# Kernel tuning notes

Hardware: AMD Instinct MI355X
Metric: run time of the kernel (lower is better)

The kernel has to match this reference:

```python
import jax, jax.numpy as jnp
import numpy as np

K = 32  # neighbors per sampled point
EPS = 1e-5

def _layernorm(h, g, b):
    mu = jnp.mean(h, axis=-1, keepdims=True)
    var = jnp.mean((h - mu) ** 2, axis=-1, keepdims=True)
    return (h - mu) * jax.lax.rsqrt(var + EPS) * g + b


def setup_inputs() -> dict:
    key = jax.random.key(0)
    ks = jax.random.split(key, 20)
    N, M, D_IN, D_T = 32768, 4096, 64, 128
    s = lambda k, *sh: jax.random.normal(k, sh, dtype=jnp.float32) * 0.05
    inp = {
        "x": jax.random.normal(ks[0], (N, D_IN), dtype=jnp.float32),
        "pos": jax.random.normal(ks[1], (N, 3), dtype=jnp.float32),
        "idx": jax.random.randint(ks[2], (M,), 0, N, dtype=jnp.int32),
        "batch": jnp.zeros((N,), dtype=jnp.int32),
        # PointNetConv MLP [67 -> 128 -> 256] (ReLU after first layer only)
        "W1": s(ks[3], D_IN + 3, 128), "b1": jnp.zeros((128,), jnp.float32),
        "W2": s(ks[4], 128, 256),     "b2": jnp.zeros((256,), jnp.float32),
        # feature_reduction Linear(256, 128)
        "Wr": s(ks[5], 256, D_T), "br": jnp.zeros((D_T,), jnp.float32),
        # MultiheadAttention(128, 4)
        "in_proj_w": s(ks[6], D_T, 3 * D_T), "in_proj_b": jnp.zeros((3 * D_T,), jnp.float32),
        "out_proj_w": s(ks[7], D_T, D_T),    "out_proj_b": jnp.zeros((D_T,), jnp.float32),
        # transformer MLP [128 -> 256 -> 128]
        "Wm1": s(ks[8], D_T, 2 * D_T), "bm1": jnp.zeros((2 * D_T,), jnp.float32),
        "Wm2": s(ks[9], 2 * D_T, D_T), "bm2": jnp.zeros((D_T,), jnp.float32),
        # layer norms
        "g1": jnp.ones((D_T,), jnp.float32), "beta1": jnp.zeros((D_T,), jnp.float32),
        "g2": jnp.ones((D_T,), jnp.float32), "beta2": jnp.zeros((D_T,), jnp.float32),
    }
    return inp


def _forward(x, pos, idx, batch, W1, b1, W2, b2, Wr, br,
             in_proj_w, in_proj_b, out_proj_w, out_proj_b,
             Wm1, bm1, Wm2, bm2, g1, beta1, g2, beta2):
    q_pos = pos[idx]                                    # [M,3]
    # KNN: k nearest source points for each sampled (dst) point
    d2 = (jnp.sum(q_pos ** 2, -1, keepdims=True)
          - 2.0 * (q_pos @ pos.T)
          + jnp.sum(pos ** 2, -1)[None, :])             # [M,N]
    _, col = jax.lax.top_k(-d2, K)                      # [M,K] source indices
    # PointNetConv message: nn([x_j, pos_j - pos_i]), max-aggregate per dst
    x_j = x[col]                                        # [M,K,64]
    rel = pos[col] - q_pos[:, None, :]                  # [M,K,3]
    feat = jnp.concatenate([x_j, rel], axis=-1)         # [M,K,67]
    h = jax.nn.relu(feat @ W1 + b1) @ W2 + b2           # [M,K,256]
    agg = jnp.max(h, axis=1)                            # [M,256]
    xt = agg @ Wr + br                                  # [M,128]
    # TransformerBlock: x.view(M,1,128) -> MHA over seq len M, batch 1
    M, D = xt.shape
    H = 4
    Dh = D // H
    qkv = xt @ in_proj_w + in_proj_b                    # [M,3D]
    qh, kh, vh = [t.reshape(M, H, Dh) for t in jnp.split(qkv, 3, axis=-1)]
    scores = jnp.einsum('qhd,khd->hqk', qh, kh) / np.sqrt(Dh)
    attn = jax.nn.softmax(scores, axis=-1)
    att = jnp.einsum('hqk,khd->qhd', attn, vh).reshape(M, D)
    att = att @ out_proj_w + out_proj_b
    xt = _layernorm(xt + att, g1, beta1)
    mlp = jax.nn.relu(xt @ Wm1 + bm1) @ Wm2 + bm2
    xt = _layernorm(xt + mlp, g2, beta2)
    return xt, q_pos, batch[idx]


def reference(x, pos, idx, batch, W1, b1, W2, b2, Wr, br,
              in_proj_w, in_proj_b, out_proj_w, out_proj_b,
              Wm1, bm1, Wm2, bm2, g1, beta1, g2, beta2):
    return _forward(x, pos, idx, batch, W1, b1, W2, b2, Wr, br,
                    in_proj_w, in_proj_b, out_proj_w, out_proj_b,
                    Wm1, bm1, Wm2, bm2, g1, beta1, g2, beta2)
```

## Files before the change

kernel.cpp:

```cpp
#include <hip/hip_runtime.h>
#include <hip/hip_bf16.h>

#define DEV static __device__ __forceinline__

typedef __attribute__((ext_vector_type(8))) short          s16x8;
typedef __attribute__((ext_vector_type(8))) unsigned short u16x8;
typedef __attribute__((ext_vector_type(4))) float          f32x4;
typedef __attribute__((ext_vector_type(4))) unsigned int   u32x4;

#define MFMA16(A,B,C) __builtin_amdgcn_mfma_f32_16x16x32_bf16((A),(B),(C),0,0,0)

DEV unsigned short f2bf(float f) {
  unsigned int u = __builtin_bit_cast(unsigned int, f);
  u += 0x7fffu + ((u >> 16) & 1u);
  return (unsigned short)(u >> 16);
}

#define QSCL 0.25503562201f

#define GRID_LO  (-5.0f)
#define GRID_IH  (3.2f)

DEV int cellc(float v) {
  int c = (int)floorf((v - GRID_LO) * GRID_IH);
  return min(31, max(0, c));
}

constexpr size_t OFF_POS4  = 0;
constexpr size_t OFF_COL   = 524288;
constexpr size_t OFF_W1T   = 1048576;
constexpr size_t OFF_W2T   = OFF_W1T  + 24576;
constexpr size_t OFF_WRT   = OFF_W2T  + 65536;
constexpr size_t OFF_WQKVT = OFF_WRT  + 65536;
constexpr size_t OFF_WOUTT = OFF_WQKVT+ 98304;
constexpr size_t OFF_WM1T  = OFF_WOUTT+ 32768;
constexpr size_t OFF_WM2T  = OFF_WM1T + 65536;
constexpr size_t OFF_H     = OFF_WM2T + 65536;
constexpr size_t OFF_SPOS    = OFF_H;
constexpr size_t OFF_CELLCNT = OFF_H + 524288;
constexpr size_t OFF_CELLDSC = OFF_H + 655360;
constexpr size_t OFF_FILL    = OFF_H + 917504;
constexpr size_t OFF_PO      = OFF_H;
constexpr size_t OFF_PL      = OFF_H + 16777216;
constexpr size_t OFF_AGG   = OFF_H    + 33554432;
constexpr size_t OFF_XT0   = OFF_AGG  + 4194304;
constexpr size_t OFF_QKV   = OFF_XT0  + 2097152;
constexpr size_t OFF_ATT   = OFF_QKV  + 6291456;
constexpr size_t OFF_PRE   = OFF_ATT  + 2097152;
constexpr size_t OFF_XT1   = OFF_PRE  + 2097152;
constexpr size_t OFF_MLP1  = OFF_XT1  + 2097152;
constexpr size_t OFF_SBIAS = OFF_MLP1 + 4194304;

__global__ __launch_bounds__(256) void zero_k(int* __restrict__ p) {
  p[blockIdx.x * 256 + threadIdx.x] = 0;
}

__global__ __launch_bounds__(256) void prep_k(
    const float* __restrict__ pos, const float* __restrict__ W1,
    const float* __restrict__ W2, const float* __restrict__ Wr,
    const float* __restrict__ ipw, const float* __restrict__ ipb,
    const float* __restrict__ opw,
    const float* __restrict__ Wm1, const float* __restrict__ Wm2,
    float4* __restrict__ pos4, unsigned short* __restrict__ w1t,
    unsigned short* __restrict__ w2t, unsigned short* __restrict__ wrt,
    unsigned short* __restrict__ wqkvt, unsigned short* __restrict__ woutt,
    unsigned short* __restrict__ wm1t, unsigned short* __restrict__ wm2t,
    int* __restrict__ cellcnt, float* __restrict__ sbias) {
  int T = blockIdx.x * 256 + threadIdx.x;
  if (T < 32768) {
    float px = pos[T*3], py = pos[T*3+1], pz = pos[T*3+2];
    pos4[T] = make_float4(px, py, pz, 0.f);
    int cid = (cellc(pz)*32 + cellc(py))*32 + cellc(px);
    atomicAdd(&cellcnt[cid], 1);
    return;
  }
  T -= 32768;
  if (T < 128*96)  { int n=T/96,  k=T%96;  w1t[T]  = f2bf(k < 67 ? W1[k*128+n] : 0.f); return; }
  T -= 128*96;
  if (T < 256*128) { int n=T/128, k=T%128; w2t[T]  = f2bf(W2[k*256+n]);  return; }
  T -= 256*128;
  if (T < 128*256) { int n=T/256, k=T%256; wrt[T]  = f2bf(Wr[k*128+n]);  return; }
  T -= 128*256;
  if (T < 384*128) { int n=T/128, k=T%128;
                     float v = ipw[k*384+n];
                     if (n < 128) v *= QSCL;
                     wqkvt[T]= f2bf(v); return; }
  T -= 384*128;
  if (T < 128*128) { int n=T/128, k=T%128; woutt[T]= f2bf(opw[k*128+n]); return; }
  T -= 128*128;
  if (T < 256*128) { int n=T/128, k=T%128; wm1t[T] = f2bf(Wm1[k*256+n]); return; }
  T -= 256*128;
  if (T < 128*256) { int n=T/256, k=T%256; wm2t[T] = f2bf(Wm2[k*128+n]); return; }
  T -= 128*256;
  if (T < 384) { sbias[T] = ipb[T] * (T < 128 ? QSCL : 1.f); return; }
}

__global__ __launch_bounds__(1024) void prefix_k(const int* __restrict__ cnt,
                                                 int2* __restrict__ desc,
                                                 int* __restrict__ fill) {
  __shared__ int wsum[16];
  const int tid = threadIdx.x, lane = tid & 63, w = tid >> 6;
  int loc[32]; int s = 0;
  #pragma unroll
  for (int i = 0; i < 32; ++i) { loc[i] = cnt[tid*32 + i]; s += loc[i]; }
  int sc = s;
  #pragma unroll
  for (int off = 1; off < 64; off <<= 1) {
    int v = __shfl_up(sc, off);
    if (lane >= off) sc += v;
  }
  if (lane == 63) wsum[w] = sc;
  __syncthreads();
  if (tid == 0) {
    int run = 0;
    #pragma unroll
    for (int i = 0; i < 16; ++i) { int v = wsum[i]; wsum[i] = run; run += v; }
  }
  __syncthreads();
  int base = wsum[w] + (sc - s);
  #pragma unroll
  for (int i = 0; i < 32; ++i) {
    int c = tid*32 + i;
    desc[c] = make_int2(base, loc[i]);
    fill[c] = base;
    base += loc[i];
  }
}

__global__ __launch_bounds__(256) void scatter_k(const float4* __restrict__ pos4,
                                                 int* __restrict__ fill,
                                                 float4* __restrict__ spos) {
  int T = blockIdx.x * 256 + threadIdx.x;
  float4 p = pos4[T];
  int cid = (cellc(p.z)*32 + cellc(p.y))*32 + cellc(p.x);
  int slot = atomicAdd(&fill[cid], 1);
  spos[slot] = make_float4(p.x, p.y, p.z, __int_as_float(T));
}

#define KNN_CAP  320
#define KNN_TRIG 192
#define KNN_KEEP 33
#define KNN_INF  3e37f

__global__ __launch_bounds__(256) void knn_k(
    const float4* __restrict__ spos, const int2* __restrict__ desc,
    const float4* __restrict__ pos4, const int* __restrict__ idx,
    int* __restrict__ col,
    float* __restrict__ outqpos, float* __restrict__ outbatch) {
  __shared__ float bufd[4][KNN_CAP];
  __shared__ int   bufi[4][KNN_CAP];
  __shared__ int   shist[4][64];
  __shared__ int2  segs[4][128];
  const int tid = threadIdx.x, lane = tid & 63, w = tid >> 6;
  const unsigned long long ltmask = (1ull << lane) - 1ull;

  const int q = blockIdx.x * 4 + w;
  const int iq = idx[q];
  const float4 qp = pos4[iq];
  const float qx = qp.x, qy = qp.y, qz = qp.z;
  const int cx0 = cellc(qx), cy0 = cellc(qy), cz0 = cellc(qz);

  float t = KNN_INF;
  int cnt = 0;

  auto compact = [&]() {
    int c_ = min(cnt, KNN_CAP);
    float vd[5]; int vi[5], bs[5]; bool okv[5];
    float dmax = 1e-30f;
    #pragma unroll
    for (int s = 0; s < 5; ++s) {
      int o2 = s*64 + lane;
      okv[s] = o2 < c_;
      vd[s] = okv[s] ? bufd[w][o2] : 0.f;
      vi[s] = okv[s] ? bufi[w][o2] : 0;
      dmax = fmaxf(dmax, vd[s]);
    }
    #pragma unroll
    for (int off = 1; off < 64; off <<= 1) dmax = fmaxf(dmax, __shfl_xor(dmax, off));
    float scale = 63.99f / dmax;
    shist[w][lane] = 0;
    #pragma unroll
    for (int s = 0; s < 5; ++s) {
      bs[s] = okv[s] ? min(63, (int)(vd[s] * scale)) : 64;
      if (okv[s]) atomicAdd(&shist[w][bs[s]], 1);
    }
    int h = shist[w][lane];
    #pragma unroll
    for (int off = 1; off < 64; off <<= 1) {
      int v = __shfl_up(h, off);
      if (lane >= off) h += v;
    }
    unsigned long long mk = __ballot(h >= KNN_KEEP);
    int E = mk ? (__ffsll((long long)mk) - 1) : 63;
    int base = 0;
    #pragma unroll
    for (int s = 0; s < 5; ++s) {
      bool keep = okv[s] && bs[s] <= E;
      unsigned long long km = __ballot(keep);
      int pp = base + (int)__popcll(km & ltmask);
      if (keep) { bufd[w][pp] = vd[s]; bufi[w][pp] = vi[s]; }
      base += (int)__popcll(km);
    }
    cnt = base;
    t = fminf(t, (float)(E + 1) / scale);
  };

  auto scan_rows = [&](int knew, int kold) {
    const int S = 2*knew + 1;
    const int NR = S*S;
    const float invS = 1.f / (float)S;
    for (int r0 = 0; r0 < NR; r0 += 64) {
      int r = r0 + lane;
      bool v = r < NR;
      int dz = (int)((float)r * invS);
      int rem = r - dz*S;
      if (rem < 0) { dz--; rem += S; } else if (rem >= S) { dz++; rem -= S; }
      int ccz = cz0 + dz - knew, ccy = cy0 + rem - knew;
      bool rowok = v && ccz >= 0 && ccz < 32 && ccy >= 0 && ccy < 32;
      bool inner = kold >= 0 && abs(dz - knew) <= kold && abs(rem - knew) <= kold;
      int cbase = (ccz*32 + ccy) * 32;
      int sL = 0, lL = 0, sR = 0, lR = 0;
      if (rowok) {
        int xa = max(cx0 - knew, 0);
        int xb = inner ? (cx0 - kold - 1) : min(cx0 + knew, 31);
        if (xa <= xb) {
          int2 d0 = desc[cbase + xa];
          int2 d1 = desc[cbase + xb];
          sL = d0.x; lL = d1.x + d1.y - d0.x;
        }
        if (inner) {
          int xa2 = cx0 + kold + 1, xb2 = min(cx0 + knew, 31);
          if (xa2 <= xb2 && xa2 >= 0) {
            int2 d0 = desc[cbase + xa2];
            int2 d1 = desc[cbase + xb2];
            sR = d0.x; lR = d1.x + d1.y - d0.x;
          }
        }
      }
      int cumL = lL;
      #pragma unroll
      for (int off = 1; off < 64; off <<= 1) {
        int vv = __shfl_up(cumL, off);
        if (lane >= off) cumL += vv;
      }
      int sumL = __shfl(cumL, 63);
      int cumR = lR;
      #pragma unroll
      for (int off = 1; off < 64; off <<= 1) {
        int vv = __shfl_up(cumR, off);
        if (lane >= off) cumR += vv;
      }
      int sumR = __shfl(cumR, 63);
      segs[w][lane]      = make_int2(sL, cumL - lL);
      segs[w][64 + lane] = make_int2(sR, sumL + cumR - lR);
      const int total = sumL + sumR;

      for (int b = 0; b < total; b += 320) {
        float d2v[5]; int piv[5]; bool hv[5];
        #pragma unroll
        for (int s5 = 0; s5 < 5; ++s5) {
          int p = b + s5*64 + lane;
          bool act = p < total;
          hv[s5] = false; d2v[s5] = 0.f; piv[s5] = 0;
          if (act) {
            int lo = 0;
            #pragma unroll
            for (int st = 64; st > 0; st >>= 1)
              if (segs[w][lo + st].y <= p) lo += st;
            int2 e = segs[w][lo];
            float4 pt = spos[e.x + (p - e.y)];
            float ddx = qx-pt.x, ddy = qy-pt.y, ddz = qz-pt.z;
            float d2 = ddx*ddx + ddy*ddy + ddz*ddz;
            d2v[s5] = d2; piv[s5] = __float_as_int(pt.w);
            hv[s5] = d2 < t;
          }
        }
        #pragma unroll
        for (int s5 = 0; s5 < 5; ++s5) {
          unsigned long long hm = __ballot(hv[s5]);
          if (hm) {
            int pp = cnt + (int)__popcll(hm & ltmask);
            if (hv[s5] && pp < KNN_CAP) { bufd[w][pp] = d2v[s5]; bufi[w][pp] = piv[s5]; }
            cnt += (int)__popcll(hm);
            if (cnt >= KNN_TRIG) compact();
          }
        }
      }
    }
  };

  auto bound32 = [&]() -> float {
    int c_ = min(cnt, KNN_CAP);
    float vv[5]; bool okv[5];
    float dmax = 1e-30f;
    #pragma unroll
    for (int s = 0; s < 5; ++s) {
      int o2 = s*64 + lane;
      okv[s] = o2 < c_;
      vv[s] = okv[s] ? bufd[w][o2] : 0.f;
      dmax = fmaxf(dmax, vv[s]);
    }
    #pragma unroll
    for (int off = 1; off < 64; off <<= 1) dmax = fmaxf(dmax, __shfl_xor(dmax, off));
    float scale = 63.99f / dmax;
    shist[w][lane] = 0;
    #pragma unroll
    for (int s = 0; s < 5; ++s)
      if (okv[s]) atomicAdd(&shist[w][min(63, (int)(vv[s] * scale))], 1);
    int h = shist[w][lane];
    #pragma unroll
    for (int off = 1; off < 64; off <<= 1) {
      int v = __shfl_up(h, off);
      if (lane >= off) h += v;
    }
    unsigned long long m = __ballot(h >= 32);
    int E = m ? (__ffsll((long long)m) - 1) : 63;
    return (float)(E + 1) / scale;
  };

  int kcur = 1;
  scan_rows(1, -1);
  for (int it = 0; it < 64; ++it) {
    if (cnt >= 32) {
      float t32u = bound32();
      t = fminf(t, t32u);
      int kneed = (int)(__builtin_sqrtf(t32u) * GRID_IH) + 1;
      if (kneed <= kcur || kcur >= 31) break;
      int knew = min(kneed, 31);
      scan_rows(knew, kcur);
      kcur = knew;
    } else {
      if (kcur >= 31) break;
      int knew = min(kcur + (cnt == 0 ? 2 : 1), 31);
      scan_rows(knew, kcur);
      kcur = knew;
    }
  }

  {
    int c_ = min(cnt, KNN_CAP);
    float vd[5]; int vi[5], bs[5]; bool okf[5];
    float dmax = 1e-30f;
    #pragma unroll
    for (int s = 0; s < 5; ++s) {
      int o2 = s*64 + lane;
      okf[s] = o2 < c_;
      vd[s] = okf[s] ? bufd[w][o2] : KNN_INF;
      vi[s] = okf[s] ? bufi[w][o2] : 0;
      dmax = fmaxf(dmax, okf[s] ? vd[s] : 0.f);
    }
    #pragma unroll
    for (int off = 1; off < 64; off <<= 1) dmax = fmaxf(dmax, __shfl_xor(dmax, off));
    float sc64 = 63.99f / dmax;
    shist[w][lane] = 0;
    #pragma unroll
    for (int s = 0; s < 5; ++s) {
      bs[s] = okf[s] ? min(63, (int)(vd[s] * sc64)) : 64;
      if (okf[s]) atomicAdd(&shist[w][bs[s]], 1);
    }
    int h = shist[w][lane];
    #pragma unroll
    for (int off = 1; off < 64; off <<= 1) {
      int v = __shfl_up(h, off);
      if (lane >= off) h += v;
    }
    unsigned long long m = __ballot(h >= 32);
    int E = m ? (__ffsll((long long)m) - 1) : 63;
    int c0 = (E > 0) ? __shfl(h, E - 1) : 0;
    int base = 0;
    #pragma unroll
    for (int s = 0; s < 5; ++s) {
      bool wr = okf[s] && (bs[s] < E);
      unsigned long long km = __ballot(wr);
      int pp = base + (int)__popcll(km & ltmask);
      if (wr) col[q*32 + pp] = vi[s];
      base += (int)__popcll(km);
    }
    #pragma unroll
    for (int s = 0; s < 5; ++s)
      if (!(okf[s] && bs[s] == E)) vd[s] = KNN_INF;
    int r = 32 - c0;
    #pragma unroll 1
    for (int kk = 0; kk < r; ++kk) {
      float bd = vd[0]; int bi = vi[0]; int bc = lane*8;
      #pragma unroll
      for (int s = 1; s < 5; ++s)
        if (vd[s] < bd) { bd = vd[s]; bi = vi[s]; bc = lane*8 + s; }
      #pragma unroll
      for (int off = 1; off < 64; off <<= 1) {
        float od = __shfl_xor(bd, off);
        int   oi = __shfl_xor(bi, off);
        int   oc = __shfl_xor(bc, off);
        if (od < bd || (od == bd && oc < bc)) { bd = od; bi = oi; bc = oc; }
      }
      if ((bc >> 3) == lane) {
        int sl = bc & 7;
        #pragma unroll
        for (int s = 0; s < 5; ++s) if (sl == s) vd[s] = KNN_INF;
      }
      if (lane == 0) col[q*32 + c0 + kk] = bi;
    }
  }
  if (lane == 0) {
    outqpos[q*3+0] = qx; outqpos[q*3+1] = qy; outqpos[q*3+2] = qz;
    outbatch[q] = 0.f;
  }
}

#define LA1(r,c) S[(r)*104 + (c)]
#define LB1(r,c) S[13312 + (r)*104 + (c)]
#define HB(r,c)  S[(r)*136 + (c)]
#define W2C(r,c) S[17408 + (r)*136 + (c)]

__global__ __launch_bounds__(256) void conv_k(
    const float* __restrict__ x, const float4* __restrict__ pos4,
    const int* __restrict__ idx, const int* __restrict__ col,
    const unsigned short* __restrict__ w1t, const float* __restrict__ b1,
    const unsigned short* __restrict__ w2t, const float* __restrict__ b2,
    float* __restrict__ agg) {
  __shared__ __align__(16) unsigned short S[26624];
  __shared__ int   sci[128];
  __shared__ float sqp[4][3];
  const int tid = threadIdx.x, lane = tid & 63, w = tid >> 6;
  const int wm = w >> 1, wn = w & 1;
  const int m0 = blockIdx.x * 4;

  if (tid < 128) sci[tid] = col[m0*32 + tid];
  if (tid >= 128 && tid < 132) {
    int m = m0 + tid - 128;
    float4 p = pos4[idx[m]];
    sqp[tid-128][0] = p.x; sqp[tid-128][1] = p.y; sqp[tid-128][2] = p.z;
  }
  #pragma unroll
  for (int rnd = 0; rnd < 6; ++rnd) {
    int e = (rnd*256 + tid) * 8;
    int n = e / 96, k = e % 96;
    *(u16x8*)&LB1(n, k) = *(const u16x8*)&w1t[e];
  }
  __syncthreads();

  {
    int r = tid >> 1, half = tid & 1;
    int ci = sci[r];
    const float* src = x + (size_t)ci*64 + half*32;
    #pragma unroll
    for (int c = 0; c < 4; ++c) {
      float4 va = ((const float4*)src)[c*2], vb = ((const float4*)src)[c*2+1];
      u16x8 v;
      v[0]=f2bf(va.x); v[1]=f2bf(va.y); v[2]=f2bf(va.z); v[3]=f2bf(va.w);
      v[4]=f2bf(vb.x); v[5]=f2bf(vb.y); v[6]=f2bf(vb.z); v[7]=f2bf(vb.w);
      *(u16x8*)&LA1(r, half*32 + c*8) = v;
    }
  }
  if (tid < 128) {
    int r = tid, g = r >> 5;
    float4 p = pos4[sci[r]];
    u16x8 z;
    #pragma unroll
    for (int e = 0; e < 8; ++e) z[e] = 0;
    u16x8 v0 = z;
    v0[0] = f2bf(p.x - sqp[g][0]); v0[1] = f2bf(p.y - sqp[g][1]); v0[2] = f2bf(p.z - sqp[g][2]);
    *(u16x8*)&LA1(r, 64) = v0;
    #pragma unroll
    for (int c = 1; c < 5; ++c) *(u16x8*)&LA1(r, 64 + c*8) = z;
  }
  __syncthreads();

  f32x4 acc[4][4];
  #pragma unroll
  for (int nf = 0; nf < 4; ++nf) {
    float bv = b1[wn*64 + nf*16 + (lane & 15)];
    #pragma unroll
    for (int mf = 0; mf < 4; ++mf) acc[mf][nf] = f32x4{bv, bv, bv, bv};
  }
  #pragma unroll
  for (int kc = 0; kc < 3; ++kc) {
    s16x8 af[4], bf_[4];
    #pragma unroll
    for (int mf = 0; mf < 4; ++mf)
      af[mf] = *(const s16x8*)&LA1(wm*64 + mf*16 + (lane&15), kc*32 + (lane>>4)*8);
    #pragma unroll
    for (int nf = 0; nf < 4; ++nf)
      bf_[nf] = *(const s16x8*)&LB1(wn*64 + nf*16 + (lane&15), kc*32 + (lane>>4)*8);
    #pragma unroll
    for (int mf = 0; mf < 4; ++mf)
      #pragma unroll
      for (int nf = 0; nf < 4; ++nf)
        acc[mf][nf] = MFMA16(af[mf], bf_[nf], acc[mf][nf]);
  }
  __syncthreads();

  #pragma unroll
  for (int mf = 0; mf < 4; ++mf)
    #pragma unroll
    for (int nf = 0; nf < 4; ++nf)
      #pragma unroll
      for (int j = 0; j < 4; ++j) {
        int rloc = wm*64 + mf*16 + ((lane>>4)<<2) + j;
        int cloc = wn*64 + nf*16 + (lane & 15);
        HB(rloc, cloc) = f2bf(fmaxf(acc[mf][nf][j], 0.f));
      }
  {
    int r2 = tid >> 2, kq = (tid & 3) * 32;
    const unsigned short* src = w2t + (size_t)r2*128 + kq;
    #pragma unroll
    for (int c = 0; c < 4; ++c)
      *(u16x8*)&W2C(r2, kq + c*8) = *(const u16x8*)&src[c*8];
  }
  __syncthreads();

  #pragma unroll 1
  for (int nc = 0; nc < 4; ++nc) {
    f32x4 acc2[2][4];
    #pragma unroll
    for (int nf = 0; nf < 4; ++nf) {
      float bv = b2[nc*64 + nf*16 + (lane & 15)];
      acc2[0][nf] = f32x4{bv, bv, bv, bv};
      acc2[1][nf] = f32x4{bv, bv, bv, bv};
    }
    #pragma unroll
    for (int ks = 0; ks < 4; ++ks) {
      s16x8 af[2], bf_[4];
      #pragma unroll
      for (int mf = 0; mf < 2; ++mf)
        af[mf] = *(const s16x8*)&HB(w*32 + mf*16 + (lane&15), ks*32 + (lane>>4)*8);
      #pragma unroll
      for (int nf = 0; nf < 4; ++nf)
        bf_[nf] = *(const s16x8*)&W2C(nf*16 + (lane&15), ks*32 + (lane>>4)*8);
      #pragma unroll
      for (int mf = 0; mf < 2; ++mf)
        #pragma unroll
        for (int nf = 0; nf < 4; ++nf)
          acc2[mf][nf] = MFMA16(af[mf], bf_[nf], acc2[mf][nf]);
    }
    #pragma unroll
    for (int nf = 0; nf < 4; ++nf) {
      float mx = acc2[0][nf][0];
      #pragma unroll
      for (int j = 1; j < 4; ++j) mx = fmaxf(mx, acc2[0][nf][j]);
      #pragma unroll
      for (int j = 0; j < 4; ++j) mx = fmaxf(mx, acc2[1][nf][j]);
      mx = fmaxf(mx, __shfl_xor(mx, 16));
      mx = fmaxf(mx, __shfl_xor(mx, 32));
      if (lane < 16) agg[(size_t)(m0 + w)*256 + nc*64 + nf*16 + lane] = mx;
    }
    if (nc < 3) {
      __syncthreads();
      int r2 = tid >> 2, kq = (tid & 3) * 32;
      const unsigned short* src = w2t + (size_t)((nc+1)*64 + r2)*128 + kq;
      #pragma unroll
      for (int c = 0; c < 4; ++c)
        *(u16x8*)&W2C(r2, kq + c*8) = *(const u16x8*)&src[c*8];
      __syncthreads();
    }
  }
}

template<int KFULL, int NFULL, bool RELU, bool HAS_RES, bool OBF16>
__global__ __launch_bounds__(256) void gemm_k(
    const float* __restrict__ A, const unsigned short* __restrict__ Bt,
    const float* __restrict__ bias, const float* __restrict__ res,
    float* __restrict__ out) {
  __shared__ unsigned short lA[64][72];
  __shared__ unsigned short lB[64][72];
  const int tid = threadIdx.x, lane = tid & 63, w = tid >> 6;
  const int m0 = blockIdx.x * 64, n0 = blockIdx.y * 64;

  f32x4 acc[4];
  #pragma unroll
  for (int nf = 0; nf < 4; ++nf) {
    float bv = bias[n0 + nf*16 + (lane & 15)];
    acc[nf] = f32x4{bv, bv, bv, bv};
  }

  for (int kb = 0; kb < KFULL; kb += 64) {
    __syncthreads();
    {
      int r = tid >> 2, kq = (tid & 3) * 16;
      const float* src = A + (size_t)(m0 + r)*KFULL + kb + kq;
      #pragma unroll
      for (int c = 0; c < 2; ++c) {
        float4 va = ((const float4*)src)[c*2], vb = ((const float4*)src)[c*2+1];
        u16x8 v;
        v[0]=f2bf(va.x); v[1]=f2bf(va.y); v[2]=f2bf(va.z); v[3]=f2bf(va.w);
        v[4]=f2bf(vb.x); v[5]=f2bf(vb.y); v[6]=f2bf(vb.z); v[7]=f2bf(vb.w);
        *(u16x8*)&lA[r][kq + c*8] = v;
      }
      const unsigned short* srcb = Bt + (size_t)(n0 + r)*KFULL + kb + kq;
      #pragma unroll
      for (int c = 0; c < 2; ++c)
        *(u16x8*)&lB[r][kq + c*8] = *(const u16x8*)&srcb[c*8];
    }
    __syncthreads();
    #pragma unroll
    for (int ks = 0; ks < 2; ++ks) {
      s16x8 af = *(const s16x8*)&lA[w*16 + (lane&15)][ks*32 + (lane>>4)*8];
      s16x8 bf_[4];
      #pragma unroll
      for (int nf = 0; nf < 4; ++nf)
        bf_[nf] = *(const s16x8*)&lB[nf*16 + (lane&15)][ks*32 + (lane>>4)*8];
      #pragma unroll
      for (int nf = 0; nf < 4; ++nf)
        acc[nf] = MFMA16(af, bf_[nf], acc[nf]);
    }
  }
  #pragma unroll
  for (int nf = 0; nf < 4; ++nf)
    #pragma unroll
    for (int j = 0; j < 4; ++j) {
      int row = m0 + w*16 + ((lane>>4)<<2) + j;
      int colg = n0 + nf*16 + (lane & 15);
      float v = acc[nf][j];
      if (HAS_RES) v += res[(size_t)row*NFULL + colg];
      if (RELU)    v = fmaxf(v, 0.f);
      if (OBF16) ((unsigned short*)out)[(size_t)row*NFULL + colg] = f2bf(v);
      else       out[(size_t)row*NFULL + colg] = v;
    }
}

__global__ __launch_bounds__(256) void attn_k(
    const unsigned short* __restrict__ qkvb,
    float* __restrict__ po, float* __restrict__ pl) {
  __shared__ unsigned short lK[128][40];
  __shared__ unsigned short lV[32][136];
  const int tid = threadIdx.x, lane = tid & 63, w = tid >> 6;
  const int hh = blockIdx.y, sp = blockIdx.z;
  const int qr = blockIdx.x * 64 + w * 16;
  const int g = lane >> 4, q = lane & 15;

  s16x8 qf = *(const s16x8*)&qkvb[(size_t)(qr + q)*384 + hh*32 + g*8];

  f32x4 o[2];
  o[0] = f32x4{0.f,0.f,0.f,0.f}; o[1] = f32x4{0.f,0.f,0.f,0.f};
  float lrun = 0.f;

  const int srcA = q | ((2*(g & 1)) << 4);
  const int srcB = srcA + 16;
  const bool hi = (g >> 1) != 0;

  for (int kt = sp*4; kt < sp*4 + 4; ++kt) {
    const int k0 = kt * 128;
    __syncthreads();
    {
      int key = tid >> 1, d0 = (tid & 1) * 16;
      const unsigned short* src = qkvb + (size_t)(k0 + key)*384 + 128 + hh*32 + d0;
      *(u16x8*)&lK[key][d0]     = *(const u16x8*)&src[0];
      *(u16x8*)&lK[key][d0 + 8] = *(const u16x8*)&src[8];
    }
    {
      int kp = tid & 63, gg = tid >> 6;
      const unsigned short* s0 = qkvb + (size_t)(k0 + 2*kp)*384 + 256 + hh*32 + gg*8;
      u16x8 e0 = *(const u16x8*)s0;
      u16x8 e1 = *(const u16x8*)(s0 + 384);
      #pragma unroll
      for (int d = 0; d < 8; ++d) {
        unsigned int pkk = (unsigned int)e0[d] | ((unsigned int)e1[d] << 16);
        *(unsigned int*)&lV[gg*8 + d][2*kp] = pkk;
      }
    }
    __syncthreads();

    unsigned int pk[8][2];
    float ps = 0.f;
    #pragma unroll
    for (int nf = 0; nf < 8; ++nf) {
      s16x8 kf = *(const s16x8*)&lK[nf*16 + q][g*8];
      f32x4 c = MFMA16(kf, qf, (f32x4{0.f,0.f,0.f,0.f}));
      float p0 = exp2f(c[0]), p1 = exp2f(c[1]);
      float p2 = exp2f(c[2]), p3 = exp2f(c[3]);
      ps += (p0 + p1) + (p2 + p3);
      unsigned int u0 = __builtin_bit_cast(unsigned int, p0) + 0x8000u;
      unsigned int u1 = __builtin_bit_cast(unsigned int, p1) + 0x8000u;
      unsigned int u2 = __builtin_bit_cast(unsigned int, p2) + 0x8000u;
      unsigned int u3 = __builtin_bit_cast(unsigned int, p3) + 0x8000u;
      pk[nf][0] = (u0 >> 16) | (u1 & 0xffff0000u);
      pk[nf][1] = (u2 >> 16) | (u3 & 0xffff0000u);
    }
    ps += __shfl_xor(ps, 16);
    ps += __shfl_xor(ps, 32);
    lrun += ps;

    #pragma unroll
    for (int kc = 0; kc < 4; ++kc) {
      unsigned int a0 = (unsigned int)__shfl((int)pk[2*kc][0],   srcA);
      unsigned int b0 = (unsigned int)__shfl((int)pk[2*kc+1][0], srcA);
      unsigned int a1 = (unsigned int)__shfl((int)pk[2*kc][1],   srcA);
      unsigned int b1 = (unsigned int)__shfl((int)pk[2*kc+1][1], srcA);
      unsigned int a2 = (unsigned int)__shfl((int)pk[2*kc][0],   srcB);
      unsigned int b2 = (unsigned int)__shfl((int)pk[2*kc+1][0], srcB);
      unsigned int a3 = (unsigned int)__shfl((int)pk[2*kc][1],   srcB);
      unsigned int b3 = (unsigned int)__shfl((int)pk[2*kc+1][1], srcB);
      u32x4 wv;
      wv[0] = hi ? b0 : a0; wv[1] = hi ? b1 : a1;
      wv[2] = hi ? b2 : a2; wv[3] = hi ? b3 : a3;
      s16x8 pa = __builtin_bit_cast(s16x8, wv);
      #pragma unroll
      for (int df = 0; df < 2; ++df) {
        s16x8 vf = *(const s16x8*)&lV[df*16 + q][kc*32 + g*8];
        o[df] = MFMA16(pa, vf, o[df]);
      }
    }
  }
  #pragma unroll
  for (int df = 0; df < 2; ++df)
    #pragma unroll
    for (int j = 0; j < 4; ++j) {
      int row = qr + g*4 + j;
      po[((size_t)sp*4096 + row)*128 + hh*32 + df*16 + q] = o[df][j];
    }
  if (lane < 16)
    pl[((sp*4 + hh) << 12) + qr + lane] = lrun;
}

__global__ __launch_bounds__(256) void attc_k(
    const float* __restrict__ po, const float* __restrict__ pl,
    float* __restrict__ att) {
  int T = blockIdx.x * 256 + threadIdx.x;
  int qrow = T >> 7, c = T & 127, hh = c >> 5;
  float l = 0.f, ov = 0.f;
  #pragma unroll
  for (int s = 0; s < 8; ++s) {
    l  += pl[((s*4 + hh) << 12) + qrow];
    ov += po[((size_t)s*4096 + qrow)*128 + c];
  }
  att[(size_t)qrow*128 + c] = ov / l;
}

__global__ __launch_bounds__(256) void ln_k(const float* __restrict__ in,
    const float* __restrict__ g, const float* __restrict__ b,
    float* __restrict__ out) {
  const int tid = threadIdx.x, lane = tid & 63, w = tid >> 6;
  const int row = blockIdx.x * 4 + w;
  float v0 = in[(size_t)row*128 + lane];
  float v1 = in[(size_t)row*128 + 64 + lane];
  float s = v0 + v1;
  #pragma unroll
  for (int off = 1; off < 64; off <<= 1) s += __shfl_xor(s, off);
  float mu = s * (1.f/128.f);
  float d0 = v0 - mu, d1 = v1 - mu;
  float qq = d0*d0 + d1*d1;
  #pragma unroll
  for (int off = 1; off < 64; off <<= 1) qq += __shfl_xor(qq, off);
  float r = rsqrtf(qq * (1.f/128.f) + 1e-5f);
  out[(size_t)row*128 + lane]      = d0 * r * g[lane]      + b[lane];
  out[(size_t)row*128 + 64 + lane] = d1 * r * g[64 + lane] + b[64 + lane];
}

extern "C" void kernel_launch(void* const* d_in, const int* in_sizes, int n_in,
                              void* d_out, int out_size, void* d_ws, size_t ws_size,
                              hipStream_t stream) {
  const float* x    = (const float*)d_in[0];
  const float* pos  = (const float*)d_in[1];
  const int*   idx  = (const int*)d_in[2];
  const float* W1   = (const float*)d_in[4];
  const float* b1   = (const float*)d_in[5];
  const float* W2   = (const float*)d_in[6];
  const float* b2   = (const float*)d_in[7];
  const float* Wr   = (const float*)d_in[8];
  const float* br   = (const float*)d_in[9];
  const float* ipw  = (const float*)d_in[10];
  const float* ipb  = (const float*)d_in[11];
  const float* opw  = (const float*)d_in[12];
  const float* opb  = (const float*)d_in[13];
  const float* Wm1  = (const float*)d_in[14];
  const float* bm1  = (const float*)d_in[15];
  const float* Wm2  = (const float*)d_in[16];
  const float* bm2  = (const float*)d_in[17];
  const float* g1   = (const float*)d_in[18];
  const float* be1  = (const float*)d_in[19];
  const float* g2   = (const float*)d_in[20];
  const float* be2  = (const float*)d_in[21];
  float* out = (float*)d_out;
  char* ws = (char*)d_ws;

  float4*         pos4  = (float4*)(ws + OFF_POS4);
  int*            colp  = (int*)(ws + OFF_COL);
  unsigned short* w1t   = (unsigned short*)(ws + OFF_W1T);
  unsigned short* w2t   = (unsigned short*)(ws + OFF_W2T);
  unsigned short* wrt   = (unsigned short*)(ws + OFF_WRT);
  unsigned short* wqkvt = (unsigned short*)(ws + OFF_WQKVT);
  unsigned short* woutt = (unsigned short*)(ws + OFF_WOUTT);
  unsigned short* wm1t  = (unsigned short*)(ws + OFF_WM1T);
  unsigned short* wm2t  = (unsigned short*)(ws + OFF_WM2T);
  float4* sposp = (float4*)(ws + OFF_SPOS);
  int*    ccnt  = (int*)(ws + OFF_CELLCNT);
  int2*   cdesc = (int2*)(ws + OFF_CELLDSC);
  int*    cfill = (int*)(ws + OFF_FILL);
  float*  pop   = (float*)(ws + OFF_PO);
  float*  plp   = (float*)(ws + OFF_PL);
  float* aggp  = (float*)(ws + OFF_AGG);
  float* xt0p  = (float*)(ws + OFF_XT0);
  unsigned short* qkvb = (unsigned short*)(ws + OFF_QKV);
  float* attp  = (float*)(ws + OFF_ATT);
  float* prep_ = (float*)(ws + OFF_PRE);
  float* xt1p  = (float*)(ws + OFF_XT1);
  float* mlp1p = (float*)(ws + OFF_MLP1);
  float* sbias = (float*)(ws + OFF_SBIAS);

  zero_k<<<128, 256, 0, stream>>>(ccnt);
  prep_k<<<946, 256, 0, stream>>>(pos, W1, W2, Wr, ipw, ipb, opw, Wm1, Wm2,
                                  pos4, w1t, w2t, wrt, wqkvt, woutt, wm1t, wm2t,
                                  ccnt, sbias);
  prefix_k<<<1, 1024, 0, stream>>>(ccnt, cdesc, cfill);
  scatter_k<<<128, 256, 0, stream>>>(pos4, cfill, sposp);
  knn_k<<<1024, 256, 0, stream>>>(sposp, cdesc, pos4, idx, colp,
                                  out + 524288, out + 536576);
  conv_k<<<1024, 256, 0, stream>>>(x, pos4, idx, colp, w1t, b1, w2t, b2, aggp);
  gemm_k<256, 128, false, false, false><<<dim3(64, 2), 256, 0, stream>>>(aggp, wrt, br, nullptr, xt0p);
  gemm_k<128, 384, false, false, true><<<dim3(64, 6), 256, 0, stream>>>(xt0p, wqkvt, sbias, nullptr, (float*)qkvb);
  attn_k<<<dim3(64, 4, 8), 256, 0, stream>>>(qkvb, pop, plp);
  attc_k<<<2048, 256, 0, stream>>>(pop, plp, attp);
  gemm_k<128, 128, false, true, false><<<dim3(64, 2), 256, 0, stream>>>(attp, woutt, opb, xt0p, prep_);
  ln_k<<<1024, 256, 0, stream>>>(prep_, g1, be1, xt1p);
  gemm_k<128, 256, true, false, false><<<dim3(64, 4), 256, 0, stream>>>(xt1p, wm1t, bm1, nullptr, mlp1p);
  gemm_k<256, 128, false, true, false><<<dim3(64, 2), 256, 0, stream>>>(mlp1p, wm2t, bm2, xt1p, prep_);
  ln_k<<<1024, 256, 0, stream>>>(prep_, g2, be2, out);
}
```

Before: 166.4 us.

## Fuse attention split-combine, output projection, residual and layernorm into GEMM epilogue

Adds a gemmln_k kernel that computes a full 128-wide output row tile per block, so the residual add and layernorm run in the GEMM epilogue. The attention partial-sum combine is folded into the A-tile load as well. This replaces six launches (attc_k, two gemm_k, two ln_k) with two, and removes the intermediate att and pre buffers with their global round trips. The cost is only 64 blocks per launch, which leaves much of the GPU idle, and more registers per thread.

After: 168.1 us. About the same (+1.0%).

```diff
diff --git a/kernel.cpp b/kernel.cpp
--- a/kernel.cpp
+++ b/kernel.cpp
@@ -618,6 +618,117 @@
     }
 }
 
+template<int KFULL, bool COMBINE>
+__global__ __launch_bounds__(256) void gemmln_k(
+    const float* __restrict__ A,
+    const float* __restrict__ po, const float* __restrict__ pl,
+    const unsigned short* __restrict__ Bt, const float* __restrict__ bias,
+    const float* __restrict__ res,
+    const float* __restrict__ gam, const float* __restrict__ bet,
+    float* __restrict__ out) {
+  __shared__ unsigned short lA[64][KFULL + 8];
+  __shared__ unsigned short lB[128][72];
+  const int tid = threadIdx.x, lane = tid & 63, w = tid >> 6;
+  const int g = lane >> 4, ln_ = lane & 15;
+  const int m0 = blockIdx.x * 64;
+
+  if (COMBINE) {
+    int r = tid >> 2, hh = tid & 3;
+    int row = m0 + r;
+    float lsum = 0.f;
+    #pragma unroll
+    for (int s = 0; s < 8; ++s) lsum += pl[((s*4 + hh) << 12) + row];
+    float inv = 1.f / lsum;
+    const float4* pob = (const float4*)po;
+    #pragma unroll
+    for (int c2 = 0; c2 < 4; ++c2) {
+      float ax=0,ay=0,az=0,aw=0, bx=0,by=0,bz=0,bw=0;
+      #pragma unroll
+      for (int s = 0; s < 8; ++s) {
+        size_t b = ((size_t)s*4096 + row)*32 + hh*8 + c2*2;
+        float4 x0 = pob[b], x1 = pob[b+1];
+        ax+=x0.x; ay+=x0.y; az+=x0.z; aw+=x0.w;
+        bx+=x1.x; by+=x1.y; bz+=x1.z; bw+=x1.w;
+      }
+      u16x8 v;
+      v[0]=f2bf(ax*inv); v[1]=f2bf(ay*inv); v[2]=f2bf(az*inv); v[3]=f2bf(aw*inv);
+      v[4]=f2bf(bx*inv); v[5]=f2bf(by*inv); v[6]=f2bf(bz*inv); v[7]=f2bf(bw*inv);
+      *(u16x8*)&lA[r][hh*32 + c2*8] = v;
+    }
+  } else {
+    int r = tid >> 2, kq = (tid & 3) * (KFULL/4);
+    const float* src = A + (size_t)(m0 + r)*KFULL + kq;
+    #pragma unroll
+    for (int c = 0; c < KFULL/32; ++c) {
+      float4 va = ((const float4*)src)[c*2], vb = ((const float4*)src)[c*2+1];
+      u16x8 v;
+      v[0]=f2bf(va.x); v[1]=f2bf(va.y); v[2]=f2bf(va.z); v[3]=f2bf(va.w);
+      v[4]=f2bf(vb.x); v[5]=f2bf(vb.y); v[6]=f2bf(vb.z); v[7]=f2bf(vb.w);
+      *(u16x8*)&lA[r][kq + c*8] = v;
+    }
+  }
+
+  float bv[8], gm[8], bt[8];
+  #pragma unroll
+  for (int nf = 0; nf < 8; ++nf) {
+    bv[nf] = bias[nf*16 + ln_];
+    gm[nf] = gam[nf*16 + ln_];
+    bt[nf] = bet[nf*16 + ln_];
+  }
+  f32x4 acc[8];
+  #pragma unroll
+  for (int nf = 0; nf < 8; ++nf) acc[nf] = f32x4{bv[nf], bv[nf], bv[nf], bv[nf]};
+
+  for (int kb = 0; kb < KFULL; kb += 64) {
+    __syncthreads();
+    {
+      int r = tid >> 1, kq = (tid & 1) * 32;
+      const unsigned short* src = Bt + (size_t)r*KFULL + kb + kq;
+      #pragma unroll
+      for (int c = 0; c < 4; ++c)
+        *(u16x8*)&lB[r][kq + c*8] = *(const u16x8*)&src[c*8];
+    }
+    __syncthreads();
+    #pragma unroll
+    for (int ks = 0; ks < 2; ++ks) {
+      s16x8 af = *(const s16x8*)&lA[w*16 + ln_][kb + ks*32 + g*8];
+      s16x8 bf_[8];
+      #pragma unroll
+      for (int nf = 0; nf < 8; ++nf)
+        bf_[nf] = *(const s16x8*)&lB[nf*16 + ln_][ks*32 + g*8];
+      #pragma unroll
+      for (int nf = 0; nf < 8; ++nf)
+        acc[nf] = MFMA16(af, bf_[nf], acc[nf]);
+    }
+  }
+
+  #pragma unroll
+  for (int j = 0; j < 4; ++j) {
+    int row = m0 + w*16 + g*4 + j;
+    float sm = 0.f;
+    #pragma unroll
+    for (int nf = 0; nf < 8; ++nf) {
+      acc[nf][j] += res[(size_t)row*128 + nf*16 + ln_];
+      sm += acc[nf][j];
+    }
+    sm += __shfl_xor(sm, 1); sm += __shfl_xor(sm, 2);
+    sm += __shfl_xor(sm, 4); sm += __shfl_xor(sm, 8);
+    float mu = sm * 0.0078125f;
+    float qv = 0.f;
+    #pragma unroll
+    for (int nf = 0; nf < 8; ++nf) {
+      float d = acc[nf][j] - mu;
+      qv += d*d;
+    }
+    qv += __shfl_xor(qv, 1); qv += __shfl_xor(qv, 2);
+    qv += __shfl_xor(qv, 4); qv += __shfl_xor(qv, 8);
+    float rr = rsqrtf(qv * 0.0078125f + 1e-5f);
+    #pragma unroll
+    for (int nf = 0; nf < 8; ++nf)
+      out[(size_t)row*128 + nf*16 + ln_] = (acc[nf][j] - mu) * rr * gm[nf] + bt[nf];
+  }
+}
+
 __global__ __launch_bounds__(256) void attn_k(
     const unsigned short* __restrict__ qkvb,
     float* __restrict__ po, float* __restrict__ pl) {
@@ -710,40 +821,6 @@
     }
   if (lane < 16)
     pl[((sp*4 + hh) << 12) + qr + lane] = lrun;
-}
-
-__global__ __launch_bounds__(256) void attc_k(
-    const float* __restrict__ po, const float* __restrict__ pl,
-    float* __restrict__ att) {
-  int T = blockIdx.x * 256 + threadIdx.x;
-  int qrow = T >> 7, c = T & 127, hh = c >> 5;
-  float l = 0.f, ov = 0.f;
-  #pragma unroll
-  for (int s = 0; s < 8; ++s) {
-    l  += pl[((s*4 + hh) << 12) + qrow];
-    ov += po[((size_t)s*4096 + qrow)*128 + c];
-  }
-  att[(size_t)qrow*128 + c] = ov / l;
-}
-
-__global__ __launch_bounds__(256) void ln_k(const float* __restrict__ in,
-    const float* __restrict__ g, const float* __restrict__ b,
-    float* __restrict__ out) {
-  const int tid = threadIdx.x, lane = tid & 63, w = tid >> 6;
-  const int row = blockIdx.x * 4 + w;
-  float v0 = in[(size_t)row*128 + lane];
-  float v1 = in[(size_t)row*128 + 64 + lane];
-  float s = v0 + v1;
-  #pragma unroll
-  for (int off = 1; off < 64; off <<= 1) s += __shfl_xor(s, off);
-  float mu = s * (1.f/128.f);
-  float d0 = v0 - mu, d1 = v1 - mu;
-  float qq = d0*d0 + d1*d1;
-  #pragma unroll
-  for (int off = 1; off < 64; off <<= 1) qq += __shfl_xor(qq, off);
-  float r = rsqrtf(qq * (1.f/128.f) + 1e-5f);
-  out[(size_t)row*128 + lane]      = d0 * r * g[lane]      + b[lane];
-  out[(size_t)row*128 + 64 + lane] = d1 * r * g[64 + lane] + b[64 + lane];
 }
 
 extern "C" void kernel_launch(void* const* d_in, const int* in_sizes, int n_in,
@@ -791,8 +868,6 @@
   float* aggp  = (float*)(ws + OFF_AGG);
   float* xt0p  = (float*)(ws + OFF_XT0);
   unsigned short* qkvb = (unsigned short*)(ws + OFF_QKV);
-  float* attp  = (float*)(ws + OFF_ATT);
-  float* prep_ = (float*)(ws + OFF_PRE);
   float* xt1p  = (float*)(ws + OFF_XT1);
   float* mlp1p = (float*)(ws + OFF_MLP1);
   float* sbias = (float*)(ws + OFF_SBIAS);
@@ -809,10 +884,7 @@
   gemm_k<256, 128, false, false, false><<<dim3(64, 2), 256, 0, stream>>>(aggp, wrt, br, nullptr, xt0p);
   gemm_k<128, 384, false, false, true><<<dim3(64, 6), 256, 0, stream>>>(xt0p, wqkvt, sbias, nullptr, (float*)qkvb);
   attn_k<<<dim3(64, 4, 8), 256, 0, stream>>>(qkvb, pop, plp);
-  attc_k<<<2048, 256, 0, stream>>>(pop, plp, attp);
-  gemm_k<128, 128, false, true, false><<<dim3(64, 2), 256, 0, stream>>>(attp, woutt, opb, xt0p, prep_);
-  ln_k<<<1024, 256, 0, stream>>>(prep_, g1, be1, xt1p);
+  gemmln_k<128, true><<<64, 256, 0, stream>>>(nullptr, pop, plp, woutt, opb, xt0p, g1, be1, xt1p);
   gemm_k<128, 256, true, false, false><<<dim3(64, 4), 256, 0, stream>>>(xt1p, wm1t, bm1, nullptr, mlp1p);
-  gemm_k<256, 128, false, true, false><<<dim3(64, 2), 256, 0, stream>>>(mlp1p, wm2t, bm2, xt1p, prep_);
-  ln_k<<<1024, 256, 0, stream>>>(prep_, g2, be2, out);
-}
+  gemmln_k<256, false><<<64, 256, 0, stream>>>(mlp1p, nullptr, nullptr, wm2t, bm2, xt1p, g2, be2, out);
+}
```
